# Performance work log

Hardware: AMD Instinct MI355X
Metric: run time of the kernel (lower is better)

Reference implementation:

```python
import jax, jax.numpy as jnp
import numpy as np

B_SZ, L, D_MODEL = 2, 2048, 2048
INTER, HEADS, P, N, G, K = 4096, 64, 64, 128, 1, 4
CONV_DIM = INTER + 2 * G * N
EPS = 1e-5


def silu(x):
    return x * jax.nn.sigmoid(x)


def softplus_thresh(x, threshold=10.0):
    # matches source: where(x < thr, log(1+exp(x)), x)
    return jnp.where(x < threshold, jnp.log1p(jnp.exp(jnp.minimum(x, threshold))), x)


def setup_inputs() -> dict:
    key = jax.random.key(0)
    ks = jax.random.split(key, 8)
    s = 0.02
    return {
        "hidden_states": jax.random.normal(ks[0], (B_SZ, L, D_MODEL), jnp.float32),
        "W_z": jax.random.normal(ks[1], (D_MODEL, INTER), jnp.float32) * s,
        "W_xBC": jax.random.normal(ks[2], (D_MODEL, CONV_DIM), jnp.float32) * s,
        "W_dt": jax.random.normal(ks[3], (D_MODEL, HEADS), jnp.float32) * s,
        "conv_w": jax.random.normal(ks[4], (CONV_DIM, K), jnp.float32) * 0.1,
        "conv_b": jnp.zeros((CONV_DIM,), jnp.float32),
        "dt_bias": jax.random.uniform(ks[5], (HEADS,), jnp.float32, -2.0, 0.0),
        "A_log": jnp.log(jnp.arange(1, HEADS + 1, dtype=jnp.float32)),
        "D": jnp.ones((HEADS,), jnp.float32),
        "norm_w": jnp.ones((INTER,), jnp.float32),
        "W_out": jax.random.normal(ks[6], (INTER, D_MODEL), jnp.float32) * s,
    }


def reference(hidden_states, W_z, W_xBC, W_dt, conv_w, conv_b, dt_bias, A_log, D, norm_w, W_out):
    b, l, _ = hidden_states.shape
    Hg = HEADS // G  # heads per group

    gate = hidden_states @ W_z                      # [b,l,INTER]
    xBC = hidden_states @ W_xBC                     # [b,l,CONV_DIM]
    dt = softplus_thresh(hidden_states @ W_dt + dt_bias)  # [b,l,H]

    # causal depthwise conv1d + silu (padding=K-1, truncated to seq_len)
    xp = jnp.pad(xBC, ((0, 0), (K - 1, 0), (0, 0)))
    kern = jnp.transpose(conv_w)[:, None, :]        # [K,1,CONV_DIM] (WIO)
    xBC = jax.lax.conv_general_dilated(
        xp, kern, (1,), 'VALID',
        dimension_numbers=('NWC', 'WIO', 'NWC'),
        feature_group_count=CONV_DIM)
    xBC = silu(xBC + conv_b)

    gns = G * N
    x = xBC[..., :INTER].reshape(b, l, G, Hg, P)
    Bm = xBC[..., INTER:INTER + gns].reshape(b, l, G, N)
    Cm = xBC[..., INTER + gns:].reshape(b, l, G, N)

    A = -jnp.exp(A_log)                             # [H]
    dA = jnp.exp(dt * A).reshape(b, l, G, Hg)       # [b,l,G,Hg]
    dtx = dt.reshape(b, l, G, Hg)[..., None] * x    # [b,l,G,Hg,P]

    def step(state, inp):
        dA_t, dtx_t, B_t, C_t = inp
        # state: [b,G,Hg,P,N]
        state = state * dA_t[..., None, None] + dtx_t[..., None] * B_t[:, :, None, None, :]
        y_t = jnp.einsum('bghpn,bgn->bghp', state, C_t)
        return state, y_t

    xs = (jnp.moveaxis(dA, 1, 0), jnp.moveaxis(dtx, 1, 0),
          jnp.moveaxis(Bm, 1, 0), jnp.moveaxis(Cm, 1, 0))
    state0 = jnp.zeros((b, G, Hg, P, N), jnp.float32)
    _, ys = jax.lax.scan(step, state0, xs)          # [l,b,G,Hg,P]
    y = jnp.moveaxis(ys, 0, 1) + D.reshape(G, Hg)[..., None] * x
    scan_out = y.reshape(b, l, INTER)

    # gated RMSNorm within groups
    hs = scan_out.reshape(b, l, G, INTER // G).astype(jnp.float32)
    gt = gate.reshape(b, l, G, INTER // G).astype(jnp.float32)
    hs = hs * silu(gt)
    var = jnp.mean(hs * hs, axis=-1, keepdims=True)
    hs = hs * jax.lax.rsqrt(var + EPS)
    normed = norm_w * hs.reshape(b, l, INTER)

    return normed @ W_out
```

## Files before the change

### kernel.cpp

```cpp
#include <hip/hip_runtime.h>
#include <hip/hip_bf16.h>
#include <math.h>

typedef unsigned short u16;
typedef unsigned int   u32;
typedef __attribute__((ext_vector_type(8))) short short8;
typedef __attribute__((ext_vector_type(8))) unsigned short us8;
typedef __attribute__((ext_vector_type(4))) float f32x4;

#define B_SZ     2
#define LSEQ     2048
#define DMODEL   2048
#define INTER    4096
#define HEADS    64
#define NSTATE   128
#define CONV_DIM 4352
#define XSTR     8576
#define NMAIN    8192
#define NTAILC   512
#define NTAILS   384
#define EPS      1e-5f
#define QCH      64
#define NCHUNK   (LSEQ / QCH)

__device__ __forceinline__ float bf2f(u16 u) {
    u32 v = ((u32)u) << 16;
    return __builtin_bit_cast(float, v);
}
__device__ __forceinline__ u16 f2bf(float x) {
    __hip_bfloat16 h = __float2bfloat16(x);
    return __builtin_bit_cast(u16, h);
}
__device__ __forceinline__ u32 pack2(float lo, float hi) {
    return (u32)f2bf(lo) | ((u32)f2bf(hi) << 16);
}
__device__ __forceinline__ void gl2lds16(const void* g, void* l) {
    __builtin_amdgcn_global_load_lds(
        (const __attribute__((address_space(1))) u32*)g,
        (__attribute__((address_space(3))) u32*)l, 16, 0, 0);
}

__global__ __launch_bounds__(256) void cvt_f32_bf16(
    const float* __restrict__ in, u16* __restrict__ out, int n4)
{
    int i = blockIdx.x * 256 + threadIdx.x;
    if (i >= n4) return;
    float4 v = ((const float4*)in)[i];
    ushort4 o;
    o.x = f2bf(v.x); o.y = f2bf(v.y); o.z = f2bf(v.z); o.w = f2bf(v.w);
    ((ushort4*)out)[i] = o;
}

__global__ __launch_bounds__(256) void tr_f32_bf16(
    const float* __restrict__ in, u16* __restrict__ out, int R, int C)
{
    __shared__ u16 tile[64][68];
    const int r0 = blockIdx.y * 64, c0 = blockIdx.x * 64;
    const int tr = threadIdx.x >> 4, tc = (threadIdx.x & 15) * 4;
    #pragma unroll
    for (int i = 0; i < 4; ++i) {
        int r = tr + i * 16;
        float4 v = *(const float4*)(in + (size_t)(r0 + r) * C + c0 + tc);
        tile[r][tc + 0] = f2bf(v.x);
        tile[r][tc + 1] = f2bf(v.y);
        tile[r][tc + 2] = f2bf(v.z);
        tile[r][tc + 3] = f2bf(v.w);
    }
    __syncthreads();
    #pragma unroll
    for (int i = 0; i < 4; ++i) {
        int oc = tr + i * 16;
        ushort4 o;
        o.x = tile[tc + 0][oc];
        o.y = tile[tc + 1][oc];
        o.z = tile[tc + 2][oc];
        o.w = tile[tc + 3][oc];
        *(ushort4*)(out + (size_t)(c0 + oc) * R + r0 + tc) = o;
    }
}

#define SA(c) (smem + (c) * 32768)
#define SB(c) (smem + (c) * 32768 + 16384)
#define STGA(c, q, ko) gl2lds16(gA + (size_t)((q) * 64) * lda + (ko), SA(c) + (q) * 4096 + lbase)
#define STGB(c, q, ko) gl2lds16(gB + (size_t)((q) * 64) * ldb + (ko), SB(c) + (q) * 4096 + lbase)

#define PH(mh, kk, READB, STAGES, TAIL)                                          \
  {                                                                              \
    short8 af[4];                                                                \
    _Pragma("unroll")                                                            \
    for (int i_ = 0; i_ < 4; ++i_)                                               \
      af[i_] = *(const short8*)(Ab + (wm * 128 + (mh) * 64 + i_ * 16 + lr) * 64  \
                                + ((((kk) * 4 + lq) ^ (lr & 7)) << 3));          \
    if (READB) {                                                                 \
      _Pragma("unroll")                                                          \
      for (int j_ = 0; j_ < 4; ++j_)                                             \
        bfr[kk][j_] = *(const short8*)(Bb + (wn * 64 + j_ * 16 + lr) * 64        \
                                       + ((((kk) * 4 + lq) ^ (lr & 7)) << 3));   \
    }                                                                            \
    STAGES                                                                       \
    __builtin_amdgcn_sched_barrier(0);                                           \
    __builtin_amdgcn_s_barrier();                                                \
    asm volatile("s_waitcnt lgkmcnt(0)" ::: "memory");                           \
    __builtin_amdgcn_sched_barrier(0);                                           \
    __builtin_amdgcn_s_setprio(1);                                               \
    _Pragma("unroll")                                                            \
    for (int i_ = 0; i_ < 4; ++i_)                                               \
      _Pragma("unroll")                                                          \
      for (int j_ = 0; j_ < 4; ++j_)                                             \
        acc[(mh) * 4 + i_][j_] = __builtin_amdgcn_mfma_f32_16x16x32_bf16(        \
            af[i_], bfr[kk][j_], acc[(mh) * 4 + i_][j_], 0, 0, 0);               \
    __builtin_amdgcn_s_setprio(0);                                               \
    __builtin_amdgcn_sched_barrier(0);                                           \
    TAIL                                                                         \
    __builtin_amdgcn_s_barrier();                                                \
  }

#define TILE(tt, c)                                                              \
  {                                                                              \
    const int t_ = (tt);                                                         \
    const int k1_ = (t_ + 1) << 6, k2_ = (t_ + 2) << 6;                          \
    const bool st1_ = (t_ + 1 < nt), st2_ = (t_ + 2 < nt);                       \
    const u16* Ab = SA(c); const u16* Bb = SB(c);                                \
    PH(0, 0, 1, { if (st1_) { STGA((c) ^ 1, 1, k1_); STGA((c) ^ 1, 3, k1_); } }, {}) \
    PH(1, 0, 0, { if (st1_) { STGB((c) ^ 1, 0, k1_); STGB((c) ^ 1, 1, k1_); } }, {}) \
    PH(0, 1, 1, { if (st1_) { STGB((c) ^ 1, 2, k1_); STGB((c) ^ 1, 3, k1_); } }, {}) \
    PH(1, 1, 0, { if (st2_) { STGA((c), 0, k2_); STGA((c), 2, k2_); } },         \
       { if (t_ < nt - 1) {                                                      \
           if (st2_) { asm volatile("s_waitcnt vmcnt(2)" ::: "memory"); }        \
           else      { asm volatile("s_waitcnt vmcnt(0)" ::: "memory"); } } })   \
  }

template<int OUT_BF16>
__global__ __launch_bounds__(512, 2) void gemm8(
    const u16* __restrict__ A, const u16* __restrict__ Bt, void* __restrict__ Co,
    int K, int lda, int ldb, int ldc, int Nstore)
{
    __shared__ __align__(16) u16 smem[65536];
    const int tid  = threadIdx.x;
    const int wave = tid >> 6, lane = tid & 63;
    const int wm = wave >> 2, wn = wave & 3;
    const int lr = lane & 15, lq = lane >> 4;

    const int nbx = gridDim.x;
    const int bid = blockIdx.y * nbx + blockIdx.x;
    const int nwg = nbx * gridDim.y;
    const int cpx = nwg >> 3;
    const int swz = (bid & 7) * cpx + (bid >> 3);
    const int n0 = (swz % nbx) * 256;
    const int m0 = (swz / nbx) * 256;
    const int kbase = blockIdx.z * K;

    const int srow  = tid >> 3;
    const int scb8  = ((tid & 7) ^ (srow & 7)) << 3;
    const int lbase = (tid >> 6) << 9;
    const u16* gA = A  + (size_t)(m0 + srow) * lda + kbase + scb8;
    const u16* gB = Bt + (size_t)(n0 + srow) * ldb + kbase + scb8;

    f32x4 acc[8][4];
    #pragma unroll
    for (int i = 0; i < 8; ++i)
        #pragma unroll
        for (int j = 0; j < 4; ++j) acc[i][j] = (f32x4)0.f;
    short8 bfr[2][4];

    const int nt = K >> 6;

    STGA(0, 0, 0); STGA(0, 1, 0); STGA(0, 2, 0); STGA(0, 3, 0);
    STGB(0, 0, 0); STGB(0, 1, 0); STGB(0, 2, 0); STGB(0, 3, 0);
    STGA(1, 0, 64); STGA(1, 2, 64);
    __builtin_amdgcn_sched_barrier(0);
    asm volatile("s_waitcnt vmcnt(2)" ::: "memory");
    __builtin_amdgcn_sched_barrier(0);
    __builtin_amdgcn_s_barrier();

    for (int t = 0; t < nt; t += 2) {
        TILE(t, 0)
        TILE(t + 1, 1)
    }

    const int odd = lr & 1;
    const bool wstore = (n0 + wn * 64) < Nstore;
    #pragma unroll
    for (int i = 0; i < 8; ++i)
        #pragma unroll
        for (int j = 0; j < 4; ++j) {
            float v0 = acc[i][j][0], v1 = acc[i][j][1];
            float v2 = acc[i][j][2], v3 = acc[i][j][3];
            float n0v = __shfl_xor(v0, 1), n1v = __shfl_xor(v1, 1);
            float n2v = __shfl_xor(v2, 1), n3v = __shfl_xor(v3, 1);
            int colb  = n0 + wn * 64 + j * 16 + (lr & ~1);
            int rbase = m0 + wm * 128 + i * 16 + lq * 4 + odd * 2;
            if (wstore) {
                if (OUT_BF16) {
                    u32 w0 = odd ? pack2(n2v, v2) : pack2(v0, n0v);
                    u32 w1 = odd ? pack2(n3v, v3) : pack2(v1, n1v);
                    *(u32*)((u16*)Co + (size_t)rbase * ldc + colb) = w0;
                    *(u32*)((u16*)Co + (size_t)(rbase + 1) * ldc + colb) = w1;
                } else {
                    float* Cf = (float*)Co + (size_t)blockIdx.z * 4096 * ldc;
                    float2 f0 = odd ? make_float2(n2v, v2) : make_float2(v0, n0v);
                    float2 f1 = odd ? make_float2(n3v, v3) : make_float2(v1, n1v);
                    *(float2*)(Cf + (size_t)rbase * ldc + colb) = f0;
                    *(float2*)(Cf + (size_t)(rbase + 1) * ldc + colb) = f1;
                }
            }
        }
}

__global__ __launch_bounds__(256) void tail_add(
    const float* __restrict__ Pt, u16* __restrict__ xall_)
{
    int i = blockIdx.x * 256 + threadIdx.x;
    int row = i / 96, cq = (i % 96) * 4;
    const float* p = Pt + (size_t)row * NTAILC + cq;
    const size_t zs = (size_t)4096 * NTAILC;
    float4 a = *(const float4*)(p);
    float4 b = *(const float4*)(p + zs);
    float4 c = *(const float4*)(p + 2 * zs);
    float4 d = *(const float4*)(p + 3 * zs);
    ushort4 o;
    o.x = f2bf(a.x + b.x + c.x + d.x);
    o.y = f2bf(a.y + b.y + c.y + d.y);
    o.z = f2bf(a.z + b.z + c.z + d.z);
    o.w = f2bf(a.w + b.w + c.w + d.w);
    *(ushort4*)(xall_ + (size_t)row * XSTR + NMAIN + cq) = o;
}

__global__ __launch_bounds__(256) void add2_f32(
    const float* __restrict__ a, const float* __restrict__ b,
    float* __restrict__ o, int n4)
{
    int i = blockIdx.x * 256 + threadIdx.x;
    if (i >= n4) return;
    float4 x = ((const float4*)a)[i];
    float4 y = ((const float4*)b)[i];
    x.x += y.x; x.y += y.y; x.z += y.z; x.w += y.w;
    ((float4*)o)[i] = x;
}

__global__ __launch_bounds__(256) void conv_kernel(
    const u16* __restrict__ xall, const float* __restrict__ cw,
    const float* __restrict__ cb, u16* __restrict__ xout,
    float* __restrict__ dtb, const float* __restrict__ dt_bias)
{
    int c4 = blockIdx.x * 256 + threadIdx.x;
    int bt = blockIdx.y;
    if (c4 >= CONV_DIM / 4) {
        int h = c4 - CONV_DIM / 4;
        if (h < HEADS) {
            float x = bf2f(xall[(size_t)bt * XSTR + INTER + CONV_DIM + h]) + dt_bias[h];
            dtb[bt * HEADS + h] = (x < 10.f) ? log1pf(expf(x)) : x;
        }
        return;
    }
    int c  = c4 * 4;
    int t  = bt & (LSEQ - 1);
    const u16* xi = xall + (size_t)bt * XSTR + INTER + c;
    float4 w0 = *(const float4*)(cw + (size_t)(c + 0) * 4);
    float4 w1 = *(const float4*)(cw + (size_t)(c + 1) * 4);
    float4 w2 = *(const float4*)(cw + (size_t)(c + 2) * 4);
    float4 w3 = *(const float4*)(cw + (size_t)(c + 3) * 4);
    float4 bb = *(const float4*)(cb + c);
    float a0 = bb.x, a1 = bb.y, a2 = bb.z, a3 = bb.w;
    ushort4 x0 = *(const ushort4*)(xi);
    a0 = fmaf(bf2f(x0.x), w0.w, a0); a1 = fmaf(bf2f(x0.y), w1.w, a1);
    a2 = fmaf(bf2f(x0.z), w2.w, a2); a3 = fmaf(bf2f(x0.w), w3.w, a3);
    if (t >= 1) {
        ushort4 xm = *(const ushort4*)(xi - XSTR);
        a0 = fmaf(bf2f(xm.x), w0.z, a0); a1 = fmaf(bf2f(xm.y), w1.z, a1);
        a2 = fmaf(bf2f(xm.z), w2.z, a2); a3 = fmaf(bf2f(xm.w), w3.z, a3);
    }
    if (t >= 2) {
        ushort4 xm = *(const ushort4*)(xi - 2 * XSTR);
        a0 = fmaf(bf2f(xm.x), w0.y, a0); a1 = fmaf(bf2f(xm.y), w1.y, a1);
        a2 = fmaf(bf2f(xm.z), w2.y, a2); a3 = fmaf(bf2f(xm.w), w3.y, a3);
    }
    if (t >= 3) {
        ushort4 xm = *(const ushort4*)(xi - 3 * XSTR);
        a0 = fmaf(bf2f(xm.x), w0.x, a0); a1 = fmaf(bf2f(xm.y), w1.x, a1);
        a2 = fmaf(bf2f(xm.z), w2.x, a2); a3 = fmaf(bf2f(xm.w), w3.x, a3);
    }
    ushort4 o;
    o.x = f2bf(a0 / (1.f + expf(-a0)));
    o.y = f2bf(a1 / (1.f + expf(-a1)));
    o.z = f2bf(a2 / (1.f + expf(-a2)));
    o.w = f2bf(a3 / (1.f + expf(-a3)));
    *(ushort4*)(xout + (size_t)bt * CONV_DIM + c) = o;
}

__global__ __launch_bounds__(256) void ssd_chunk_state(
    const u16* __restrict__ xc, const float* __restrict__ dtb,
    const float* __restrict__ A_log,
    u16* __restrict__ Tg, float* __restrict__ decayQ)
{
    const int bid = blockIdx.x;
    const int b = bid >> 11, h = (bid >> 5) & 63, c = bid & 31;
    const int t0 = c * QCH;
    const int tid = threadIdx.x;
    const int wave = tid >> 6, lane = tid & 63;
    const int lr = lane & 15, lq = lane >> 4;

    __shared__ __align__(16) u16 BT[128][72];
    __shared__ __align__(16) u16 XwT[64][72];
    __shared__ float sclL[QCH];

    const u16* xg = xc + (size_t)b * LSEQ * CONV_DIM;

    if (tid < 64) {
        float dtv = dtb[((size_t)b * LSEQ + t0 + tid) * HEADS + h];
        float a = -dtv * expf(A_log[h]);
        float s = a;
        #pragma unroll
        for (int off = 1; off < 64; off <<= 1) {
            float o = __shfl_up(s, off, 64);
            if (tid >= off) s += o;
        }
        float cq = __shfl(s, 63, 64);
        sclL[tid] = dtv * expf(cq - s);
        if (tid == 0) decayQ[((b * 64 + h) << 5) + c] = expf(cq);
    }
    __syncthreads();

    #pragma unroll
    for (int r = 0; r < 2; ++r) {
        int idx = tid + 256 * r;
        int j = idx >> 3, p8 = (idx & 7) * 8;
        us8 xv = *(const us8*)(xg + (size_t)(t0 + j) * CONV_DIM + h * 64 + p8);
        float scl = sclL[j];
        #pragma unroll
        for (int k = 0; k < 8; ++k)
            XwT[p8 + k][j] = f2bf(bf2f(xv[k]) * scl);
    }
    #pragma unroll
    for (int r = 0; r < 4; ++r) {
        int idx = tid + 256 * r;
        int j = idx >> 4, n8 = (idx & 15) * 8;
        us8 bv = *(const us8*)(xg + (size_t)(t0 + j) * CONV_DIM + INTER + n8);
        #pragma unroll
        for (int k = 0; k < 8; ++k)
            BT[n8 + k][j] = bv[k];
    }
    __syncthreads();

    f32x4 acc[8];
    #pragma unroll
    for (int i = 0; i < 8; ++i) acc[i] = (f32x4)0.f;
    #pragma unroll
    for (int k0 = 0; k0 < QCH; k0 += 32) {
        short8 af = *(const short8*)&XwT[wave * 16 + lr][k0 + lq * 8];
        #pragma unroll
        for (int nt = 0; nt < 8; ++nt) {
            short8 bfr = *(const short8*)&BT[nt * 16 + lr][k0 + lq * 8];
            acc[nt] = __builtin_amdgcn_mfma_f32_16x16x32_bf16(af, bfr, acc[nt], 0, 0, 0);
        }
    }
    u16* To = Tg + ((((size_t)(b * 64 + h)) * NCHUNK + c) * 64) * 128;
    #pragma unroll
    for (int nt = 0; nt < 8; ++nt)
        #pragma unroll
        for (int r = 0; r < 4; ++r)
            To[(wave * 16 + lq * 4 + r) * 128 + nt * 16 + lr] = f2bf(acc[nt][r]);
}

__global__ __launch_bounds__(256) void ssd_state_scan(
    u16* __restrict__ Tg, const float* __restrict__ decayQ)
{
    const int bh = blockIdx.x >> 2, nq = blockIdx.x & 3;
    const int tid = threadIdx.x;
    const int p = tid >> 2, nb = nq * 32 + (tid & 3) * 8;
    float S[8];
    #pragma unroll
    for (int m = 0; m < 8; ++m) S[m] = 0.f;

    for (int c = 0; c < NCHUNK; ++c) {
        u16* base = Tg + ((((size_t)bh * NCHUNK + c) * 64 + p) * 128) + nb;
        uint4 tv = *(const uint4*)base;
        uint4 sv;
        sv.x = pack2(S[0], S[1]);
        sv.y = pack2(S[2], S[3]);
        sv.z = pack2(S[4], S[5]);
        sv.w = pack2(S[6], S[7]);
        *(uint4*)base = sv;
        float dq = decayQ[(bh << 5) + c];
        const u32* w = (const u32*)&tv;
        #pragma unroll
        for (int e = 0; e < 4; ++e) {
            S[e*2]     = fmaf(dq, S[e*2],     bf2f((u16)(w[e] & 0xffffu)));
            S[e*2 + 1] = fmaf(dq, S[e*2 + 1], bf2f((u16)(w[e] >> 16)));
        }
    }
}

__global__ __launch_bounds__(256) void ssd_output(
    const u16* __restrict__ xc, const float* __restrict__ dtb,
    const float* __restrict__ A_log, const float* __restrict__ Dvec,
    const u16* __restrict__ Sg,
    u16* __restrict__ y)
{
    const int bid = blockIdx.x;
    const int b = bid >> 11, h = (bid >> 5) & 63, c = bid & 31;
    const int t0 = c * QCH;
    const int tid = threadIdx.x;
    const int wave = tid >> 6, lane = tid & 63;
    const int lr = lane & 15, lq = lane >> 4;

    __shared__ __align__(16) u16 C_lds[64][136];
    __shared__ __align__(16) u16 B_lds[64][136];
    __shared__ __align__(16) u16 S_lds[64][136];
    __shared__ __align__(16) u16 P_lds[64][72];
    __shared__ __align__(16) u16 XT[64][72];
    __shared__ float cumL[QCH], dtsL[QCH], escL[QCH];

    const u16* xg = xc + (size_t)b * LSEQ * CONV_DIM;

    if (tid < 64) {
        float dtv = dtb[((size_t)b * LSEQ + t0 + tid) * HEADS + h];
        float a = -dtv * expf(A_log[h]);
        float s = a;
        #pragma unroll
        for (int off = 1; off < 64; off <<= 1) {
            float o = __shfl_up(s, off, 64);
            if (tid >= off) s += o;
        }
        cumL[tid] = s;
        dtsL[tid] = dtv;
        escL[tid] = expf(s);
    }
    #pragma unroll
    for (int r4 = 0; r4 < 4; ++r4) {
        int idx4 = tid + 256 * r4;
        int j = idx4 >> 4, c8 = (idx4 & 15) * 8;
        *(uint4*)&B_lds[j][c8] = *(const uint4*)(xg + (size_t)(t0 + j) * CONV_DIM + INTER + c8);
        *(uint4*)&C_lds[j][c8] = *(const uint4*)(xg + (size_t)(t0 + j) * CONV_DIM + INTER + NSTATE + c8);
        *(uint4*)&S_lds[j][c8] = *(const uint4*)(Sg + ((((size_t)(b * 64 + h)) * NCHUNK + c) * 64 + j) * 128 + c8);
    }
    #pragma unroll
    for (int r = 0; r < 2; ++r) {
        int idx = tid + 256 * r;
        int j = idx >> 3, p8 = (idx & 7) * 8;
        us8 xv = *(const us8*)(xg + (size_t)(t0 + j) * CONV_DIM + h * 64 + p8);
        #pragma unroll
        for (int k = 0; k < 8; ++k)
            XT[p8 + k][j] = xv[k];
    }
    __syncthreads();

    f32x4 accG[4];
    #pragma unroll
    for (int i = 0; i < 4; ++i) accG[i] = (f32x4)0.f;
    #pragma unroll
    for (int k0 = 0; k0 < NSTATE; k0 += 32) {
        short8 af = *(const short8*)&C_lds[wave * 16 + lr][k0 + lq * 8];
        #pragma unroll
        for (int jt = 0; jt < 4; ++jt) {
            short8 bfr = *(const short8*)&B_lds[jt * 16 + lr][k0 + lq * 8];
            accG[jt] = __builtin_amdgcn_mfma_f32_16x16x32_bf16(af, bfr, accG[jt], 0, 0, 0);
        }
    }
    #pragma unroll
    for (int jt = 0; jt < 4; ++jt)
        #pragma unroll
        for (int r = 0; r < 4; ++r) {
            int ii = wave * 16 + lq * 4 + r;
            int jj = jt * 16 + lr;
            float v = (jj <= ii)
                ? accG[jt][r] * dtsL[jj] * expf(cumL[ii] - cumL[jj]) : 0.f;
            P_lds[ii][jj] = f2bf(v);
        }
    __syncthreads();

    f32x4 accY[4], accZ[4];
    #pragma unroll
    for (int i = 0; i < 4; ++i) { accY[i] = (f32x4)0.f; accZ[i] = (f32x4)0.f; }
    #pragma unroll
    for (int k0 = 0; k0 < QCH; k0 += 32) {
        short8 af = *(const short8*)&P_lds[wave * 16 + lr][k0 + lq * 8];
        #pragma unroll
        for (int pt = 0; pt < 4; ++pt) {
            short8 bfr = *(const short8*)&XT[pt * 16 + lr][k0 + lq * 8];
            accY[pt] = __builtin_amdgcn_mfma_f32_16x16x32_bf16(af, bfr, accY[pt], 0, 0, 0);
        }
    }
    #pragma unroll
    for (int k0 = 0; k0 < NSTATE; k0 += 32) {
        short8 af = *(const short8*)&C_lds[wave * 16 + lr][k0 + lq * 8];
        #pragma unroll
        for (int pt = 0; pt < 4; ++pt) {
            short8 bfr = *(const short8*)&S_lds[pt * 16 + lr][k0 + lq * 8];
            accZ[pt] = __builtin_amdgcn_mfma_f32_16x16x32_bf16(af, bfr, accZ[pt], 0, 0, 0);
        }
    }

    const float Dh = Dvec[h];
    u16* yg = y + ((size_t)b * LSEQ + t0) * XSTR + h * 64;
    #pragma unroll
    for (int pt = 0; pt < 4; ++pt)
        #pragma unroll
        for (int r = 0; r < 4; ++r) {
            int ii = wave * 16 + lq * 4 + r;
            int pp = pt * 16 + lr;
            float xv = bf2f(XT[pp][ii]);
            float o = accY[pt][r] + escL[ii] * accZ[pt][r] + Dh * xv;
            yg[(size_t)ii * XSTR + pp] = f2bf(o);
        }
}

__global__ __launch_bounds__(256) void norm_kernel(
    u16* __restrict__ xall, const float* __restrict__ w)
{
    const int row = blockIdx.x;
    const u16* yr = xall + (size_t)row * XSTR + INTER;
    u16*       gr = xall + (size_t)row * XSTR;
    const int tid = threadIdx.x;

    float v[16];
    float ss = 0.f;
    #pragma unroll
    for (int i = 0; i < 2; ++i) {
        int e0 = i * 2048 + tid * 8;
        uint4 hv4 = *(const uint4*)(yr + e0);
        uint4 gv4 = *(const uint4*)(gr + e0);
        const u16* hp = (const u16*)&hv4;
        const u16* gp = (const u16*)&gv4;
        #pragma unroll
        for (int k = 0; k < 8; ++k) {
            float hv = bf2f(hp[k]);
            float g  = bf2f(gp[k]);
            float val = hv * (g / (1.f + expf(-g)));
            v[i * 8 + k] = val;
            ss = fmaf(val, val, ss);
        }
    }
    #pragma unroll
    for (int o = 32; o > 0; o >>= 1) ss += __shfl_xor(ss, o);
    __shared__ float part[4];
    if ((tid & 63) == 0) part[tid >> 6] = ss;
    __syncthreads();
    float tot  = part[0] + part[1] + part[2] + part[3];
    float rinv = rsqrtf(tot * (1.f / INTER) + EPS);
    #pragma unroll
    for (int i = 0; i < 2; ++i) {
        int e0 = i * 2048 + tid * 8;
        float4 wa = *(const float4*)(w + e0);
        float4 wb = *(const float4*)(w + e0 + 4);
        uint4 sv;
        sv.x = pack2(wa.x * v[i*8+0] * rinv, wa.y * v[i*8+1] * rinv);
        sv.y = pack2(wa.z * v[i*8+2] * rinv, wa.w * v[i*8+3] * rinv);
        sv.z = pack2(wb.x * v[i*8+4] * rinv, wb.y * v[i*8+5] * rinv);
        sv.w = pack2(wb.z * v[i*8+6] * rinv, wb.w * v[i*8+7] * rinv);
        *(uint4*)(gr + e0) = sv;
    }
}

extern "C" void kernel_launch(void* const* d_in, const int* in_sizes, int n_in,
                              void* d_out, int out_size, void* d_ws, size_t ws_size,
                              hipStream_t stream)
{
    const float* hs      = (const float*)d_in[0];
    const float* W_z     = (const float*)d_in[1];
    const float* W_xBC   = (const float*)d_in[2];
    const float* W_dt    = (const float*)d_in[3];
    const float* conv_w  = (const float*)d_in[4];
    const float* conv_b  = (const float*)d_in[5];
    const float* dt_bias = (const float*)d_in[6];
    const float* A_log   = (const float*)d_in[7];
    const float* Dv      = (const float*)d_in[8];
    const float* norm_w  = (const float*)d_in[9];
    const float* W_out   = (const float*)d_in[10];
    float* out = (float*)d_out;
    char*  w8  = (char*)d_ws;

    u16* hs_bf  = (u16*)(w8 + 0);
    u16* Wt_all = (u16*)(w8 + 16777216);
    u16* Tbuf   = (u16*)(w8 + 0);
    float* Cpart= (float*)(w8 + 0);
    u16* Wt_out = (u16*)(w8 + 67108864);
    u16* xall   = (u16*)(w8 + 83886080);
    u16* xconv  = (u16*)(w8 + 154140672);
    float* Ptail= (float*)(w8 + 154140672);
    float* dtb  = (float*)(w8 + 189792256);
    float* dcq  = (float*)(w8 + 190840832);

    const int M = B_SZ * LSEQ;

    cvt_f32_bf16<<<(M * DMODEL / 4 + 255) / 256, 256, 0, stream>>>(hs, hs_bf, M * DMODEL / 4);
    tr_f32_bf16<<<dim3(INTER / 64,    DMODEL / 64), 256, 0, stream>>>(W_z,   Wt_all, DMODEL, INTER);
    tr_f32_bf16<<<dim3(CONV_DIM / 64, DMODEL / 64), 256, 0, stream>>>(W_xBC, Wt_all + (size_t)INTER * DMODEL, DMODEL, CONV_DIM);
    tr_f32_bf16<<<dim3(1,             DMODEL / 64), 256, 0, stream>>>(W_dt,  Wt_all + (size_t)(INTER + CONV_DIM) * DMODEL, DMODEL, 64);
    hipMemsetAsync(Wt_all + (size_t)(INTER + CONV_DIM + 64) * DMODEL, 0, (size_t)192 * DMODEL * 2, stream);
    tr_f32_bf16<<<dim3(DMODEL / 64,   INTER / 64),  256, 0, stream>>>(W_out, Wt_out, INTER, DMODEL);

    gemm8<1><<<dim3(NMAIN / 256, M / 256, 1), 512, 0, stream>>>(
        hs_bf, Wt_all, (void*)xall, DMODEL , DMODEL, DMODEL,
        XSTR , NMAIN );
    gemm8<0><<<dim3(NTAILC / 256, M / 256, 4), 512, 0, stream>>>(
        hs_bf, Wt_all + (size_t)NMAIN * DMODEL, (void*)Ptail, DMODEL / 4 ,
        DMODEL, DMODEL, NTAILC , NTAILS );
    tail_add<<<M * (NTAILS / 4) / 256, 256, 0, stream>>>(Ptail, xall);

    conv_kernel<<<dim3((CONV_DIM / 4 + 255) / 256, M), 256, 0, stream>>>(
        xall, conv_w, conv_b, xconv, dtb, dt_bias);

    ssd_chunk_state<<<B_SZ * HEADS * NCHUNK, 256, 0, stream>>>(xconv, dtb, A_log, Tbuf, dcq);
    ssd_state_scan<<<B_SZ * HEADS * 4, 256, 0, stream>>>(Tbuf, dcq);
    ssd_output<<<B_SZ * HEADS * NCHUNK, 256, 0, stream>>>(xconv, dtb, A_log, Dv, Tbuf, xall + INTER);

    norm_kernel<<<M, 256, 0, stream>>>(xall, norm_w);

    gemm8<0><<<dim3(DMODEL / 256, M / 256, 2), 512, 0, stream>>>(
        xall, Wt_out, (void*)Cpart, INTER / 2 , XSTR ,
        INTER , DMODEL , DMODEL );
    add2_f32<<<(M * DMODEL / 4 + 255) / 256, 256, 0, stream>>>(
        Cpart, Cpart + (size_t)M * DMODEL, out, M * DMODEL / 4);
}
```

Baseline: 631.1 us.

## Rework SSD chunk load/store patterns and prefetch state-scan loads

Replaces vectorized 16-byte global loads plus transposing LDS scatter with per-element scalar loads, where consecutive threads read consecutive elements and write along LDS columns, in the chunk-state and output kernels. MFMA result stores are paired through lane shuffles so each lane writes a packed 32-bit word instead of scattered 16-bit stores. The state scan prefetches the next chunk's tile before processing the current one to overlap load latency with the serial recurrence. Scalar global loads issue many more memory instructions, trading load width for fewer LDS bank conflicts.

Measured after the change: 607.6 us. -3.7%, faster.

```diff
diff --git a/kernel.cpp b/kernel.cpp
--- a/kernel.cpp
+++ b/kernel.cpp
@@ -5,7 +5,6 @@
 typedef unsigned short u16;
 typedef unsigned int   u32;
 typedef __attribute__((ext_vector_type(8))) short short8;
-typedef __attribute__((ext_vector_type(8))) unsigned short us8;
 typedef __attribute__((ext_vector_type(4))) float f32x4;
 
 #define B_SZ     2
@@ -322,23 +321,15 @@
     __syncthreads();
 
     #pragma unroll
-    for (int r = 0; r < 2; ++r) {
-        int idx = tid + 256 * r;
-        int j = idx >> 3, p8 = (idx & 7) * 8;
-        us8 xv = *(const us8*)(xg + (size_t)(t0 + j) * CONV_DIM + h * 64 + p8);
-        float scl = sclL[j];
-        #pragma unroll
-        for (int k = 0; k < 8; ++k)
-            XwT[p8 + k][j] = f2bf(bf2f(xv[k]) * scl);
-    }
-    #pragma unroll
-    for (int r = 0; r < 4; ++r) {
-        int idx = tid + 256 * r;
-        int j = idx >> 4, n8 = (idx & 15) * 8;
-        us8 bv = *(const us8*)(xg + (size_t)(t0 + j) * CONV_DIM + INTER + n8);
-        #pragma unroll
-        for (int k = 0; k < 8; ++k)
-            BT[n8 + k][j] = bv[k];
+    for (int r = 0; r < 16; ++r) {
+        int idx = tid + 256 * r, j = idx >> 6, p = idx & 63;
+        float v = bf2f(xg[(size_t)(t0 + j) * CONV_DIM + h * 64 + p]);
+        XwT[p][j] = f2bf(v * sclL[j]);
+    }
+    #pragma unroll
+    for (int r = 0; r < 32; ++r) {
+        int idx = tid + 256 * r, j = idx >> 7, n = idx & 127;
+        BT[n][j] = xg[(size_t)(t0 + j) * CONV_DIM + INTER + n];
     }
     __syncthreads();
 
@@ -355,11 +346,20 @@
         }
     }
     u16* To = Tg + ((((size_t)(b * 64 + h)) * NCHUNK + c) * 64) * 128;
-    #pragma unroll
-    for (int nt = 0; nt < 8; ++nt)
-        #pragma unroll
-        for (int r = 0; r < 4; ++r)
-            To[(wave * 16 + lq * 4 + r) * 128 + nt * 16 + lr] = f2bf(acc[nt][r]);
+    const int odd = lr & 1;
+    #pragma unroll
+    for (int nt = 0; nt < 8; ++nt) {
+        float v0 = acc[nt][0], v1 = acc[nt][1];
+        float v2 = acc[nt][2], v3 = acc[nt][3];
+        float n0v = __shfl_xor(v0, 1), n1v = __shfl_xor(v1, 1);
+        float n2v = __shfl_xor(v2, 1), n3v = __shfl_xor(v3, 1);
+        int colb  = nt * 16 + (lr & ~1);
+        int rbase = wave * 16 + lq * 4 + odd * 2;
+        u32 w0 = odd ? pack2(n2v, v2) : pack2(v0, n0v);
+        u32 w1 = odd ? pack2(n3v, v3) : pack2(v1, n1v);
+        *(u32*)(To + (size_t)rbase * 128 + colb) = w0;
+        *(u32*)(To + (size_t)(rbase + 1) * 128 + colb) = w1;
+    }
 }
 
 __global__ __launch_bounds__(256) void ssd_state_scan(
@@ -372,9 +372,11 @@
     #pragma unroll
     for (int m = 0; m < 8; ++m) S[m] = 0.f;
 
+    u16* base = Tg + (((size_t)bh * NCHUNK) * 64 + p) * 128 + nb;
+    uint4 tv = *(const uint4*)base;
     for (int c = 0; c < NCHUNK; ++c) {
-        u16* base = Tg + ((((size_t)bh * NCHUNK + c) * 64 + p) * 128) + nb;
-        uint4 tv = *(const uint4*)base;
+        uint4 tnext = tv;
+        if (c + 1 < NCHUNK) tnext = *(const uint4*)(base + 64 * 128);
         uint4 sv;
         sv.x = pack2(S[0], S[1]);
         sv.y = pack2(S[2], S[3]);
@@ -388,6 +390,8 @@
             S[e*2]     = fmaf(dq, S[e*2],     bf2f((u16)(w[e] & 0xffffu)));
             S[e*2 + 1] = fmaf(dq, S[e*2 + 1], bf2f((u16)(w[e] >> 16)));
         }
+        tv = tnext;
+        base += 64 * 128;
     }
 }
 
@@ -435,13 +439,9 @@
         *(uint4*)&S_lds[j][c8] = *(const uint4*)(Sg + ((((size_t)(b * 64 + h)) * NCHUNK + c) * 64 + j) * 128 + c8);
     }
     #pragma unroll
-    for (int r = 0; r < 2; ++r) {
-        int idx = tid + 256 * r;
-        int j = idx >> 3, p8 = (idx & 7) * 8;
-        us8 xv = *(const us8*)(xg + (size_t)(t0 + j) * CONV_DIM + h * 64 + p8);
-        #pragma unroll
-        for (int k = 0; k < 8; ++k)
-            XT[p8 + k][j] = xv[k];
+    for (int r = 0; r < 16; ++r) {
+        int idx = tid + 256 * r, j = idx >> 6, p = idx & 63;
+        XT[p][j] = xg[(size_t)(t0 + j) * CONV_DIM + h * 64 + p];
     }
     __syncthreads();
 
@@ -493,16 +493,26 @@
 
     const float Dh = Dvec[h];
     u16* yg = y + ((size_t)b * LSEQ + t0) * XSTR + h * 64;
-    #pragma unroll
-    for (int pt = 0; pt < 4; ++pt)
+    const int odd = lr & 1;
+    #pragma unroll
+    for (int pt = 0; pt < 4; ++pt) {
+        float ov[4];
         #pragma unroll
         for (int r = 0; r < 4; ++r) {
             int ii = wave * 16 + lq * 4 + r;
             int pp = pt * 16 + lr;
             float xv = bf2f(XT[pp][ii]);
-            float o = accY[pt][r] + escL[ii] * accZ[pt][r] + Dh * xv;
-            yg[(size_t)ii * XSTR + pp] = f2bf(o);
-        }
+            ov[r] = accY[pt][r] + escL[ii] * accZ[pt][r] + Dh * xv;
+        }
+        float n0v = __shfl_xor(ov[0], 1), n1v = __shfl_xor(ov[1], 1);
+        float n2v = __shfl_xor(ov[2], 1), n3v = __shfl_xor(ov[3], 1);
+        int ppb = pt * 16 + (lr & ~1);
+        int rb  = wave * 16 + lq * 4 + odd * 2;
+        u32 w0 = odd ? pack2(n2v, ov[2]) : pack2(ov[0], n0v);
+        u32 w1 = odd ? pack2(n3v, ov[3]) : pack2(ov[1], n1v);
+        *(u32*)(yg + (size_t)rb * XSTR + ppb) = w0;
+        *(u32*)(yg + (size_t)(rb + 1) * XSTR + ppb) = w1;
+    }
 }
 
 __global__ __launch_bounds__(256) void norm_kernel(
```
